# Optimization experiments

Measured on AMD Instinct MI355X. Metric: run time of the kernel, lower is better.

## Reference

```python
import jax, jax.numpy as jnp
import numpy as np

NUM_HEADS = 16


def _apply_rope(x, freqs):
    # x: (H, L, C), freqs: (L, C//2); computed in fp32, cast back to x.dtype
    xf = x.astype(jnp.float32)
    x1, x2 = jnp.split(xf, 2, axis=-1)
    f = freqs.astype(jnp.float32)[None]  # (1, L, C//2)
    cos, sin = jnp.cos(f), jnp.sin(f)
    out = jnp.concatenate((x1 * cos - x2 * sin, x1 * sin + x2 * cos), axis=-1)
    return out.astype(x.dtype)


def setup_inputs() -> dict:
    key = jax.random.key(0)
    k0, k1, k2, k3 = jax.random.split(key, 4)
    S, D, H = 4096, 1280, NUM_HEADS
    hd = D // H
    hidden_states = jax.random.normal(k0, (S, D), dtype=jnp.float32)
    cu_seqlens = jnp.array([0, 1024, 2048, 3072, 4096], dtype=jnp.int32)
    rotary_pos_emb = jax.random.normal(k1, (S, hd // 2), dtype=jnp.float32)
    scale = 1.0 / np.sqrt(D)
    w_qkv = (jax.random.normal(k2, (D, 3 * D), dtype=jnp.float32) * scale)
    b_qkv = jnp.zeros((3 * D,), dtype=jnp.float32)
    w_proj = (jax.random.normal(k3, (D, D), dtype=jnp.float32) * scale)
    b_proj = jnp.zeros((D,), dtype=jnp.float32)
    return {
        "hidden_states": hidden_states,
        "cu_seqlens": cu_seqlens,
        "rotary_pos_emb": rotary_pos_emb,
        "w_qkv": w_qkv,
        "b_qkv": b_qkv,
        "w_proj": w_proj,
        "b_proj": b_proj,
    }


def reference(hidden_states, cu_seqlens, rotary_pos_emb, w_qkv, b_qkv, w_proj, b_proj):
    S, D = hidden_states.shape
    H = NUM_HEADS
    hd = D // H
    qkv = hidden_states @ w_qkv + b_qkv            # (S, 3D)
    qkv = qkv.reshape(S, 3, H, hd).transpose(1, 2, 0, 3)  # (3, H, S, hd)
    q, k, v = qkv[0], qkv[1], qkv[2]
    q = _apply_rope(q, rotary_pos_emb)
    k = _apply_rope(k, rotary_pos_emb)
    # block-diagonal (per-segment) attention, equivalent to the per-segment loop
    seg = jnp.searchsorted(cu_seqlens, jnp.arange(S), side="right") - 1  # (S,)
    mask = seg[:, None] == seg[None, :]            # (S, S)
    scores = jnp.einsum("hqd,hkd->hqk", q, k) / np.sqrt(hd)
    scores = jnp.where(mask[None], scores, -jnp.inf)
    attn = jax.nn.softmax(scores.astype(jnp.float32), axis=-1).astype(q.dtype)
    out = jnp.einsum("hqk,hkd->qhd", attn, v).reshape(S, D)
    return out @ w_proj + b_proj
```

## Files before the change

### kernel.cpp

```cpp
#include <hip/hip_runtime.h>
#include <hip/hip_bf16.h>
#include <cstdint>

typedef __bf16 bf16x8 __attribute__((ext_vector_type(8)));
typedef __bf16 bf16x4 __attribute__((ext_vector_type(4)));
typedef short short4_ __attribute__((ext_vector_type(4)));
typedef float f32x4 __attribute__((ext_vector_type(4)));

#define SLEN 4096
#define DMODEL 1280
#define NHEADS 16
#define HD 80
#define HDP 96
#define VTILE_ELEMS 3328
#define VTILE_LDS 3584

#define GLD_LDS16(g, l)                                                        \
  __builtin_amdgcn_global_load_lds(                                            \
      (const __attribute__((address_space(1))) void*)(g),                      \
      (__attribute__((address_space(3))) void*)(l), 16, 0, 0)

#define WAIT_VMCNT(n) __builtin_amdgcn_s_waitcnt((n & 0xF) | 0x70 | 0xF00 | ((n >> 4) << 14))

__device__ __forceinline__ void transpose_body(const float* __restrict__ in,
                                               __bf16* __restrict__ out,
                                               int K, int N, int bx, int by, int t) {
  __shared__ float tile[32][33];
  int n0 = bx * 32, k0 = by * 32;
  int x = t & 31, y = t >> 5;
  for (int i = 0; i < 32; i += 8)
    tile[y + i][x] = in[(size_t)(k0 + y + i) * N + n0 + x];
  __syncthreads();
  for (int i = 0; i < 32; i += 8)
    out[(size_t)(n0 + y + i) * K + k0 + x] = (__bf16)tile[x][y + i];
}

__global__ __launch_bounds__(256) void prep(const float* __restrict__ hidden,
                                            __bf16* __restrict__ hid_b,
                                            const float* __restrict__ w_qkv,
                                            __bf16* __restrict__ wqkvT,
                                            const float* __restrict__ w_proj,
                                            __bf16* __restrict__ wprojT) {
  int bid = blockIdx.x, t = threadIdx.x;
  if (bid < 5120) {
    int i = bid * 256 + t;
    float4 v = ((const float4*)hidden)[i];
    bf16x4 o = { (__bf16)v.x, (__bf16)v.y, (__bf16)v.z, (__bf16)v.w };
    ((bf16x4*)hid_b)[i] = o;
  } else if (bid < 9920) {
    int b = bid - 5120;
    transpose_body(w_qkv, wqkvT, 1280, 3840, b % 120, b / 120, t);
  } else {
    int b = bid - 9920;
    transpose_body(w_proj, wprojT, 1280, 1280, b % 40, b / 40, t);
  }
}

template <int WMW>
__global__ __launch_bounds__(WMW * 2 * 64) void gemm_bt(const __bf16* __restrict__ A,
                                                        const __bf16* __restrict__ Bt,
                                                        const float* __restrict__ bias,
                                                        void* __restrict__ C,
                                                        int M, int N, int K, int store_bf16) {
  constexpr int BM = WMW * 64;
  constexpr int NW = WMW * 2;
  constexpr int BI = 8 / NW;
  constexpr int PW = 2 + BI;
  constexpr int ASZ = BM * 32, BSZ = 128 * 32;

  __shared__ __attribute__((aligned(16))) __bf16 As[3][ASZ];
  __shared__ __attribute__((aligned(16))) __bf16 Bs[3][BSZ];

  const int t = threadIdx.x;
  const int lane = t & 63, wave = t >> 6;
  const int quad = lane >> 4, l15 = lane & 15;
  const int wm = (wave & (WMW - 1)) * 64, wn = (wave / WMW) * 64;
  const int bm = blockIdx.x * BM, bn = blockIdx.y * 128;

  const int rs = lane >> 2, cs = (lane & 3) * 8;
  const __bf16* AgQ[2];
  const __bf16* BgQ[BI];
  int aLds[2], bLds[BI];
#pragma unroll
  for (int q = 0; q < 2; ++q) {
    int row = (wave * 2 + q) * 16;
    AgQ[q] = A + (size_t)(bm + row + rs) * K + cs;
    aLds[q] = row * 32;
  }
#pragma unroll
  for (int q = 0; q < BI; ++q) {
    int row = (wave * BI + q) * 16;
    BgQ[q] = Bt + (size_t)(bn + row + rs) * K + cs;
    bLds[q] = row * 32;
  }

  f32x4 acc[4][4] = {};
  const int niter = K >> 5;

#pragma unroll
  for (int s = 0; s < 2; ++s) {
#pragma unroll
    for (int q = 0; q < 2; ++q) GLD_LDS16(AgQ[q] + s * 32, &As[s][aLds[q]]);
#pragma unroll
    for (int q = 0; q < BI; ++q) GLD_LDS16(BgQ[q] + s * 32, &Bs[s][bLds[q]]);
  }

  int cmp = 0, stg = 2;
  for (int it = 0; it < niter; ++it) {
    const int kk = (it + 2 < niter ? it + 2 : niter - 1) * 32;
#pragma unroll
    for (int q = 0; q < 2; ++q) GLD_LDS16(AgQ[q] + kk, &As[stg][aLds[q]]);
#pragma unroll
    for (int q = 0; q < BI; ++q) GLD_LDS16(BgQ[q] + kk, &Bs[stg][bLds[q]]);
    asm volatile("" ::: "memory");
    WAIT_VMCNT(2 * PW);
    __builtin_amdgcn_s_barrier();
    asm volatile("" ::: "memory");

    bf16x8 af[4], bfr[4];
#pragma unroll
    for (int i = 0; i < 4; ++i)
      af[i] = *(const bf16x8*)&As[cmp][(wm + i * 16 + l15) * 32 + quad * 8];
#pragma unroll
    for (int j = 0; j < 4; ++j)
      bfr[j] = *(const bf16x8*)&Bs[cmp][(wn + j * 16 + l15) * 32 + quad * 8];
#pragma unroll
    for (int i = 0; i < 4; ++i)
#pragma unroll
      for (int j = 0; j < 4; ++j)
        acc[i][j] = __builtin_amdgcn_mfma_f32_16x16x32_bf16(bfr[j], af[i], acc[i][j], 0, 0, 0);

    asm volatile("" ::: "memory");
    __builtin_amdgcn_s_barrier();
    asm volatile("" ::: "memory");
    cmp = (cmp == 2) ? 0 : cmp + 1;
    stg = (stg == 2) ? 0 : stg + 1;
  }

  float4 bv[4];
#pragma unroll
  for (int j = 0; j < 4; ++j)
    bv[j] = *(const float4*)&bias[bn + wn + j * 16 + quad * 4];
#pragma unroll
  for (int i = 0; i < 4; ++i) {
    size_t row = (size_t)(bm + wm + i * 16 + l15);
#pragma unroll
    for (int j = 0; j < 4; ++j) {
      int col = bn + wn + j * 16 + quad * 4;
      const float* bp = (const float*)&bv[j];
      if (store_bf16) {
        bf16x4 ov;
#pragma unroll
        for (int r = 0; r < 4; ++r) ov[r] = (__bf16)(acc[i][j][r] + bp[r]);
        *(bf16x4*)&((__bf16*)C)[row * N + col] = ov;
      } else {
        float4 fv;
        fv.x = acc[i][j][0] + bp[0];
        fv.y = acc[i][j][1] + bp[1];
        fv.z = acc[i][j][2] + bp[2];
        fv.w = acc[i][j][3] + bp[3];
        *(float4*)&((float*)C)[row * N + col] = fv;
      }
    }
  }
}

__global__ __launch_bounds__(256) void rope_pack(const __bf16* __restrict__ qkv,
                                                 const float* __restrict__ freqs,
                                                 __bf16* __restrict__ qp,
                                                 __bf16* __restrict__ kp,
                                                 __bf16* __restrict__ vt) {
  const float QSCALE = 0.11180339887498949f * 1.44269504088896340f;
  int h = blockIdx.y;
  int s0 = blockIdx.x * 64;
  int t = threadIdx.x;
  int sp = t >> 2, l4 = t & 3;
  int s = s0 + sp;
  const __bf16* row = qkv + (size_t)s * 3840 + h * 80;
  __bf16* qo = qp + (size_t)(h * SLEN + s) * HDP;
  __bf16* ko = kp + (size_t)(h * SLEN + s) * HDP;

  __shared__ float vtile[64][81];

  for (int c = l4; c < 10; c += 4) {
    int base = (c < 5) ? c * 8 : (c - 5) * 8;
    bf16x8 xa = *(const bf16x8*)(row + base);
    bf16x8 xb = *(const bf16x8*)(row + base + 40);
    bf16x8 ya = *(const bf16x8*)(row + 1280 + base);
    bf16x8 yb = *(const bf16x8*)(row + 1280 + base + 40);
    float4 f0 = *(const float4*)(freqs + s * 40 + base);
    float4 f1 = *(const float4*)(freqs + s * 40 + base + 4);
    float fr[8] = {f0.x, f0.y, f0.z, f0.w, f1.x, f1.y, f1.z, f1.w};
    bf16x8 qv, kv;
#pragma unroll
    for (int e = 0; e < 8; ++e) {
      float cs = __builtin_cosf(fr[e]), sn = __builtin_sinf(fr[e]);
      float x1 = (float)xa[e], x2 = (float)xb[e];
      float y1 = (float)ya[e], y2 = (float)yb[e];
      float qvv, kvv;
      if (c < 5) { qvv = x1 * cs - x2 * sn; kvv = y1 * cs - y2 * sn; }
      else       { qvv = x1 * sn + x2 * cs; kvv = y1 * sn + y2 * cs; }
      qv[e] = (__bf16)(qvv * QSCALE);
      kv[e] = (__bf16)kvv;
    }
    *(bf16x8*)(qo + c * 8) = qv;
    *(bf16x8*)(ko + c * 8) = kv;
  }
  {
    bf16x8 z = {};
    if (l4 == 0) *(bf16x8*)(qo + 80) = z;
    if (l4 == 1) *(bf16x8*)(qo + 88) = z;
    if (l4 == 2) *(bf16x8*)(ko + 80) = z;
    if (l4 == 3) *(bf16x8*)(ko + 88) = z;
  }

  for (int c = l4; c < 10; c += 4) {
    bf16x8 v = *(const bf16x8*)(row + 2560 + c * 8);
#pragma unroll
    for (int e = 0; e < 8; ++e)
      vtile[sp][c * 8 + e] = (float)v[e];
  }
  __syncthreads();

  for (int idx = t; idx < 640; idx += 256) {
    int c2 = idx >= 320;
    int rem = idx - (c2 ? 320 : 0);
    int d = rem >> 2, kc = rem & 3;
    __bf16* tb = vt + (size_t)(h * (SLEN / 32) + (s0 >> 5) + c2) * VTILE_ELEMS;
    bf16x8 ov;
#pragma unroll
    for (int r = 0; r < 4; ++r) {
      ov[r]     = (__bf16)vtile[c2 * 32 + kc * 4 + r][d];
      ov[r + 4] = (__bf16)vtile[c2 * 32 + 16 + kc * 4 + r][d];
    }
    *(bf16x8*)(tb + d * 40 + kc * 8) = ov;
  }
}

__global__ __launch_bounds__(256) void flash_attn(const __bf16* __restrict__ qp,
                                                  const __bf16* __restrict__ kp,
                                                  const __bf16* __restrict__ vt,
                                                  const int* __restrict__ cu, int nseg,
                                                  __bf16* __restrict__ out) {
  const float MEXP = 16.0f;
  int h = blockIdx.y;
  int q0 = blockIdx.x * 128;
  int seg = 0;
  for (int i = 1; i < nseg; ++i)
    if (cu[i] <= q0) seg = i;
  int kstart = cu[seg], kend = cu[seg + 1];

  int t = threadIdx.x;
  int lane = t & 63, wave = t >> 6;
  int quad = lane >> 4, l15 = lane & 15;

  __shared__ __attribute__((aligned(16))) __bf16 Ks[2][64 * HDP];
  __shared__ __attribute__((aligned(16))) __bf16 Vs[2][2 * VTILE_LDS];

  bf16x8 qf[2][3];
#pragma unroll
  for (int qs = 0; qs < 2; ++qs) {
    const __bf16* qptr = qp + (size_t)(h * SLEN + q0 + wave * 32 + qs * 16 + l15) * HDP + quad * 8;
    qf[qs][0] = *(const bf16x8*)(qptr);
    qf[qs][1] = *(const bf16x8*)(qptr + 32);
    qf[qs][2] = *(const bf16x8*)(qptr + 64);
  }

  f32x4 o[2][5] = {};
  float l_p[2] = {0.f, 0.f};

  const __bf16* gK = kp + (size_t)(h * SLEN + kstart) * HDP + lane * 8;
  const __bf16* gV = vt + (size_t)(h * (SLEN / 32) + (kstart >> 5)) * VTILE_ELEMS + lane * 8;

  const int niter = (kend - kstart) >> 6;

  auto stage = [&](int kn, int buf) {
    const __bf16* ksrc = gK + (size_t)kn * (64 * HDP);
    const __bf16* vsrc = gV + (size_t)kn * (2 * VTILE_ELEMS);
#pragma unroll
    for (int i0 = 0; i0 < 7; ++i0) {
      int i = wave * 7 + i0;
      int ii = i < 26 ? i : 25;
      if (ii < 12)
        GLD_LDS16(ksrc + ii * 512, &Ks[buf][ii * 512]);
      else if (ii < 19)
        GLD_LDS16(vsrc + (ii - 12) * 512, &Vs[buf][(ii - 12) * 512]);
      else
        GLD_LDS16(vsrc + VTILE_ELEMS + (ii - 19) * 512, &Vs[buf][VTILE_LDS + (ii - 19) * 512]);
    }
  };

  stage(0, 0);

  for (int it = 0; it < niter; ++it) {
    const int cur = it & 1, nxt = cur ^ 1;
    const int kn = (it + 1 < niter) ? it + 1 : niter - 1;
    stage(kn, nxt);
    asm volatile("" ::: "memory");
    WAIT_VMCNT(7);
    __builtin_amdgcn_s_barrier();
    asm volatile("" ::: "memory");

    f32x4 sc[2][4];
#pragma unroll
    for (int nt = 0; nt < 4; ++nt) {
      sc[0][nt] = f32x4{-MEXP, -MEXP, -MEXP, -MEXP};
      sc[1][nt] = sc[0][nt];
#pragma unroll
      for (int c = 0; c < 3; ++c) {
        bf16x8 kf = *(const bf16x8*)&Ks[cur][(nt * 16 + l15) * HDP + quad * 8 + c * 32];
        sc[0][nt] = __builtin_amdgcn_mfma_f32_16x16x32_bf16(kf, qf[0][c], sc[0][nt], 0, 0, 0);
        sc[1][nt] = __builtin_amdgcn_mfma_f32_16x16x32_bf16(kf, qf[1][c], sc[1][nt], 0, 0, 0);
      }
    }

    bf16x4 pf[2][4];
#pragma unroll
    for (int qs = 0; qs < 2; ++qs)
#pragma unroll
      for (int nt = 0; nt < 4; ++nt)
#pragma unroll
        for (int r = 0; r < 4; ++r) {
          float p = __builtin_amdgcn_exp2f(sc[qs][nt][r]);
          l_p[qs] += p;
          pf[qs][nt][r] = (__bf16)p;
        }

#pragma unroll
    for (int g = 0; g < 2; ++g) {
#pragma unroll
      for (int dt = 0; dt < 5; ++dt) {
        bf16x8 vv = *(const bf16x8*)&Vs[cur][g * VTILE_LDS + (dt * 16 + l15) * 40 + quad * 8];
        bf16x4 vlo = __builtin_shufflevector(vv, vv, 0, 1, 2, 3);
        bf16x4 vhi = __builtin_shufflevector(vv, vv, 4, 5, 6, 7);
#pragma unroll
        for (int qs = 0; qs < 2; ++qs) {
          o[qs][dt] = __builtin_amdgcn_mfma_f32_16x16x16bf16_1k(
              *(short4_*)&vlo, *(short4_*)&pf[qs][g * 2], o[qs][dt], 0, 0, 0);
          o[qs][dt] = __builtin_amdgcn_mfma_f32_16x16x16bf16_1k(
              *(short4_*)&vhi, *(short4_*)&pf[qs][g * 2 + 1], o[qs][dt], 0, 0, 0);
        }
      }
    }

    asm volatile("" ::: "memory");
    __builtin_amdgcn_s_barrier();
    asm volatile("" ::: "memory");
  }

#pragma unroll
  for (int qs = 0; qs < 2; ++qs) {
    float l = l_p[qs];
    l += __shfl_xor(l, 16);
    l += __shfl_xor(l, 32);
    float rinv = 1.0f / l;
    int qrow = q0 + wave * 32 + qs * 16 + l15;
#pragma unroll
    for (int dt = 0; dt < 5; ++dt) {
      bf16x4 ov;
#pragma unroll
      for (int r = 0; r < 4; ++r)
        ov[r] = (__bf16)(o[qs][dt][r] * rinv);
      *(bf16x4*)&out[(size_t)qrow * DMODEL + h * 80 + dt * 16 + quad * 4] = ov;
    }
  }
}

extern "C" void kernel_launch(void* const* d_in, const int* in_sizes, int n_in,
                              void* d_out, int out_size, void* d_ws, size_t ws_size,
                              hipStream_t stream) {
  const float* hidden = (const float*)d_in[0];
  const int* cu       = (const int*)d_in[1];
  const float* freqs  = (const float*)d_in[2];
  const float* w_qkv  = (const float*)d_in[3];
  const float* b_qkv  = (const float*)d_in[4];
  const float* w_proj = (const float*)d_in[5];
  const float* b_proj = (const float*)d_in[6];
  float* out = (float*)d_out;

  char* ws = (char*)d_ws;
  size_t off = 0;
  auto alloc = [&](size_t bytes) {
    char* p = ws + off;
    off += (bytes + 255) & ~(size_t)255;
    return p;
  };
  __bf16* hid_b  = (__bf16*)alloc((size_t)SLEN * DMODEL * 2);
  __bf16* wqkvT  = (__bf16*)alloc((size_t)3840 * 1280 * 2);
  __bf16* wprojT = (__bf16*)alloc((size_t)1280 * 1280 * 2);
  __bf16* qkvb   = (__bf16*)alloc((size_t)SLEN * 3840 * 2);
  __bf16* qp     = (__bf16*)alloc((size_t)NHEADS * SLEN * HDP * 2);
  __bf16* kp     = (__bf16*)alloc((size_t)NHEADS * SLEN * HDP * 2 + 1024);
  __bf16* vt     = (__bf16*)alloc((size_t)NHEADS * (SLEN / 32) * VTILE_ELEMS * 2 + 1024);
  __bf16* attn   = hid_b;

  prep<<<11520, 256, 0, stream>>>(hidden, hid_b, w_qkv, wqkvT, w_proj, wprojT);
  gemm_bt<4><<<dim3(SLEN / 256, 3840 / 128), 512, 0, stream>>>(hid_b, wqkvT, b_qkv, qkvb,
                                                               SLEN, 3840, 1280, 1);
  rope_pack<<<dim3(SLEN / 64, NHEADS), 256, 0, stream>>>(qkvb, freqs, qp, kp, vt);
  int nseg = in_sizes[1] - 1;
  flash_attn<<<dim3(SLEN / 128, NHEADS), 256, 0, stream>>>(qp, kp, vt, cu, nseg, attn);
  gemm_bt<2><<<dim3(SLEN / 128, DMODEL / 128), 256, 0, stream>>>(attn, wprojT, b_proj, out,
                                                                 SLEN, DMODEL, 1280, 0);
}
```

Baseline: 240.7 us.

## Replace QKV GEMM with 256x256-tile kernel using swizzled LDS and interleaved prefetch

After: 237.0 us. No clear change (-1.5%).

```diff
diff --git a/kernel.cpp b/kernel.cpp
--- a/kernel.cpp
+++ b/kernel.cpp
@@ -21,6 +21,9 @@
       (__attribute__((address_space(3))) void*)(l), 16, 0, 0)
 
 #define WAIT_VMCNT(n) __builtin_amdgcn_s_waitcnt((n & 0xF) | 0x70 | 0xF00 | ((n >> 4) << 14))
+
+#define FENCE asm volatile("" ::: "memory")
+#define BARRIER do { FENCE; __builtin_amdgcn_s_barrier(); FENCE; } while (0)
 
 __device__ __forceinline__ void transpose_body(const float* __restrict__ in,
                                                __bf16* __restrict__ out,
@@ -56,6 +59,137 @@
   }
 }
 
+template <int I0, int J0>
+__device__ __forceinline__ void mfma16(f32x4 (&acc)[8][4], bf16x8 (&af)[4][2],
+                                       bf16x8 (&bfr)[4][2]) {
+  __builtin_amdgcn_s_setprio(1);
+#pragma unroll
+  for (int kk = 0; kk < 2; ++kk)
+#pragma unroll
+    for (int i = 0; i < 4; ++i)
+#pragma unroll
+      for (int j = 0; j < 2; ++j)
+        acc[I0 + i][J0 + j] = __builtin_amdgcn_mfma_f32_16x16x32_bf16(
+            bfr[J0 + j][kk], af[i][kk], acc[I0 + i][J0 + j], 0, 0, 0);
+  __builtin_amdgcn_s_setprio(0);
+}
+
+__global__ __launch_bounds__(512, 2) void gemm256(const __bf16* __restrict__ A,
+                                                  const __bf16* __restrict__ Bt,
+                                                  const float* __restrict__ bias,
+                                                  __bf16* __restrict__ C,
+                                                  int M, int N, int K) {
+  __shared__ __attribute__((aligned(1024))) __bf16 As[2][256 * 64];
+  __shared__ __attribute__((aligned(1024))) __bf16 Bs[2][256 * 64];
+
+  const int t = threadIdx.x;
+  const int lane = t & 63, wave = t >> 6;
+  const int quad = lane >> 4, l15 = lane & 15;
+  const int wm = wave >> 2, wn = wave & 3;
+
+  const int mb = M >> 8;
+  const int cpx = gridDim.x >> 3;
+  const int wg = (blockIdx.x & 7) * cpx + (blockIdx.x >> 3);
+  const int bm = (wg % mb) * 256, bn = (wg / mb) * 256;
+
+  const __bf16* Ab = A + (size_t)bm * K;
+  const __bf16* Bb = Bt + (size_t)bn * K;
+
+  auto stage = [&](const __bf16* g, __bf16* l, int row0, int kt) {
+    GLD_LDS16(g + (size_t)(row0 + (lane >> 3)) * K + kt * 64 +
+                  (((lane & 7) ^ ((lane >> 3) & 7)) << 3),
+              l + row0 * 64);
+  };
+  auto lda = [&](bf16x8 (&dst)[4][2], const __bf16* Al, int I0) {
+#pragma unroll
+    for (int i = 0; i < 4; ++i)
+#pragma unroll
+      for (int kk = 0; kk < 2; ++kk) {
+        int row = wm * 128 + (I0 + i) * 16 + l15;
+        int c = (kk * 64 + quad * 16) ^ ((l15 & 7) << 4);
+        dst[i][kk] = *(const bf16x8*)&Al[row * 64 + (c >> 1)];
+      }
+  };
+  auto ldb = [&](bf16x8 (&dst)[2][2], const __bf16* Bl, int J0) {
+#pragma unroll
+    for (int j = 0; j < 2; ++j)
+#pragma unroll
+      for (int kk = 0; kk < 2; ++kk) {
+        int row = wn * 64 + (J0 + j) * 16 + l15;
+        int c = (kk * 64 + quad * 16) ^ ((l15 & 7) << 4);
+        dst[j][kk] = *(const bf16x8*)&Bl[row * 64 + (c >> 1)];
+      }
+  };
+
+  const int aw = wave * 8;
+  const int be0 = (wave >> 2) * 64 + (wave & 3) * 8;
+  const int niter = K >> 6;
+
+  stage(Ab, As[0], aw, 0);        stage(Ab, As[0], 128 + aw, 0);
+  stage(Bb, Bs[0], be0, 0);       stage(Bb, Bs[0], be0 + 128, 0);
+  stage(Ab, As[0], 64 + aw, 0);   stage(Ab, As[0], 192 + aw, 0);
+  stage(Bb, Bs[0], be0 + 32, 0);  stage(Bb, Bs[0], be0 + 160, 0);
+  stage(Ab, As[1], aw, 1);        stage(Ab, As[1], 128 + aw, 1);
+  stage(Bb, Bs[1], be0, 1);       stage(Bb, Bs[1], be0 + 128, 1);
+  WAIT_VMCNT(4);
+  BARRIER;
+
+  f32x4 acc[8][4] = {};
+  bf16x8 af[4][2], bfr[4][2];
+
+  for (int it = 0; it < niter; ++it) {
+    const int cur = it & 1;
+    const __bf16* Ac = As[cur];
+    const __bf16* Bc = Bs[cur];
+    __bf16* An = As[cur ^ 1];
+    __bf16* Bn = Bs[cur ^ 1];
+    const bool p1 = it + 1 < niter, p2 = it + 2 < niter;
+
+    lda(af, Ac, 0);
+    ldb(reinterpret_cast<bf16x8(&)[2][2]>(bfr[0]), Bc, 0);
+    if (p1) { stage(Ab, An, 64 + aw, it + 1); stage(Ab, An, 192 + aw, it + 1); }
+    BARRIER;
+    mfma16<0, 0>(acc, af, bfr);
+    BARRIER;
+
+    ldb(reinterpret_cast<bf16x8(&)[2][2]>(bfr[2]), Bc, 2);
+    if (p1) { stage(Bb, Bn, be0 + 32, it + 1); stage(Bb, Bn, be0 + 160, it + 1); }
+    BARRIER;
+    mfma16<0, 2>(acc, af, bfr);
+    BARRIER;
+
+    lda(af, Ac, 4);
+    if (p2) { stage(Ab, (__bf16*)Ac, aw, it + 2); stage(Ab, (__bf16*)Ac, 128 + aw, it + 2); }
+    BARRIER;
+    mfma16<4, 0>(acc, af, bfr);
+    BARRIER;
+
+    if (p2) { stage(Bb, (__bf16*)Bc, be0, it + 2); stage(Bb, (__bf16*)Bc, be0 + 128, it + 2); }
+    BARRIER;
+    mfma16<4, 2>(acc, af, bfr);
+    WAIT_VMCNT(4);
+    BARRIER;
+  }
+
+  float4 bv[4];
+#pragma unroll
+  for (int j = 0; j < 4; ++j)
+    bv[j] = *(const float4*)&bias[bn + wn * 64 + j * 16 + quad * 4];
+#pragma unroll
+  for (int i = 0; i < 8; ++i) {
+    size_t row = (size_t)(bm + wm * 128 + i * 16 + l15);
+#pragma unroll
+    for (int j = 0; j < 4; ++j) {
+      int col = bn + wn * 64 + j * 16 + quad * 4;
+      const float* bp = (const float*)&bv[j];
+      bf16x4 ov;
+#pragma unroll
+      for (int r = 0; r < 4; ++r) ov[r] = (__bf16)(acc[i][j][r] + bp[r]);
+      *(bf16x4*)&C[row * N + col] = ov;
+    }
+  }
+}
+
 template <int WMW>
 __global__ __launch_bounds__(WMW * 2 * 64) void gemm_bt(const __bf16* __restrict__ A,
                                                         const __bf16* __restrict__ Bt,
@@ -395,8 +529,8 @@
   __bf16* attn   = hid_b;
 
   prep<<<11520, 256, 0, stream>>>(hidden, hid_b, w_qkv, wqkvT, w_proj, wprojT);
-  gemm_bt<4><<<dim3(SLEN / 256, 3840 / 128), 512, 0, stream>>>(hid_b, wqkvT, b_qkv, qkvb,
-                                                               SLEN, 3840, 1280, 1);
+  gemm256<<<dim3((SLEN / 256) * (3840 / 256)), 512, 0, stream>>>(hid_b, wqkvT, b_qkv, qkvb,
+                                                                 SLEN, 3840, 1280);
   rope_pack<<<dim3(SLEN / 64, NHEADS), 256, 0, stream>>>(qkvb, freqs, qp, kp, vt);
   int nseg = in_sizes[1] - 1;
   flash_attn<<<dim3(SLEN / 128, NHEADS), 256, 0, stream>>>(qp, kp, vt, cu, nseg, attn);
```
